# Kernel tuning notes

Hardware: AMD Instinct MI355X
Metric: run time of the kernel (lower is better)

Reference implementation:

```python
import jax, jax.numpy as jnp
import numpy as np

FP8_MAX = 448.0  # float8_e4m3fn max representable magnitude


def _fp8_quant_dequant(x, axis=-1):
    # Per-token (last-axis) dynamic scaling to e4m3, then dequantize back.
    scale = jnp.max(jnp.abs(x), axis=axis, keepdims=True) / FP8_MAX
    scale = jnp.maximum(scale, 1e-12)
    q = (x / scale).astype(jnp.float8_e4m3fn).astype(jnp.float32)
    return q * scale


def setup_inputs() -> dict:
    key = jax.random.key(0)
    k1, k2, k3, k4 = jax.random.split(key, 4)
    S, H, D, T = 64, 64, 128, 32768
    index_q = jax.random.normal(k1, (S, H, D), dtype=jnp.float32)
    index_k = jax.random.normal(k2, (T, D), dtype=jnp.float32)
    weights = jax.random.uniform(k3, (S, H), dtype=jnp.float32)
    cu_seqlen_ks = jnp.zeros((S,), dtype=jnp.int32)
    cu_seqlen_ke = jax.random.randint(k4, (S,), 1, T + 1, dtype=jnp.int32)
    return {
        "index_q": index_q,
        "index_k": index_k,
        "weights": weights,
        "cu_seqlen_ks": cu_seqlen_ks,
        "cu_seqlen_ke": cu_seqlen_ke,
    }


def reference(index_q, index_k, weights, cu_seqlen_ks, cu_seqlen_ke):
    # FP8 (e4m3) quantize-dequantize with per-token dynamic scales.
    q = _fp8_quant_dequant(index_q, axis=-1)   # [S, H, D]
    k = _fp8_quant_dequant(index_k, axis=-1)   # [T, D]
    # Index scores: relu(q.k) weighted-summed over heads -> [S, T]
    scores = jax.nn.relu(jnp.einsum("shd,td->sht", q, k))
    logits = jnp.einsum("sht,sh->st", scores, weights)
    # Ragged KV masking: query s sees kv tokens in [ks[s], ke[s]).
    t = jnp.arange(k.shape[0], dtype=jnp.int32)
    mask = (t[None, :] >= cu_seqlen_ks[:, None]) & (t[None, :] < cu_seqlen_ke[:, None])
    return jnp.where(mask, logits, -jnp.inf)
```

## Files before the change

kernel.cpp:

```cpp
#include <hip/hip_runtime.h>
#include <stdint.h>
#include <math.h>

#define NS 64
#define NH 64
#define ND 128
#define NT 32768
#define TN 256

#define MASK_VAL (-3.0e38f)

typedef __attribute__((ext_vector_type(4))) float f32x4;

__device__ __align__(16) uint8_t g_q8[NS * NH * ND];
__device__ __align__(16) uint8_t g_k8[NT * ND];
__device__ float g_wq[NS * NH];
__device__ float g_sk[NT];

__device__ __forceinline__ float wave_reduce_max(float m) {
#pragma unroll
  for (int off = 32; off >= 1; off >>= 1)
    m = fmaxf(m, __shfl_xor(m, off, 64));
  return m;
}

__device__ __forceinline__ uint32_t f32_to_e4m3(float x) {
  uint32_t u = __float_as_uint(x);
  uint32_t sign = (u >> 24) & 0x80u;
  uint32_t a = u & 0x7FFFFFFFu;
  if (a > 0x43E00000u) a = 0x43E00000u;
  uint32_t e = a >> 23;
  uint32_t code;
  if (e >= 121u) {
    uint32_t m = a & 0x7FFFFFu;
    m += 0x7FFFFu + ((m >> 20) & 1u);
    uint32_t carry = m >> 23;
    code = ((e - 120u + carry) << 3) | (carry ? 0u : ((m >> 20) & 7u));
    if (code > 0x7Eu) code = 0x7Eu;
  } else {
    code = (uint32_t)(int)rintf(__uint_as_float(a) * 512.0f);
  }
  return sign | code;
}

__global__ __launch_bounds__(256) void quant_q_kernel(
    const float* __restrict__ in, const float* __restrict__ weights) {
  int row = blockIdx.x * 4 + (threadIdx.x >> 6);
  int l = threadIdx.x & 63;
  float2 v = reinterpret_cast<const float2*>(in)[(size_t)row * 64 + l];
  float m = wave_reduce_max(fmaxf(fabsf(v.x), fabsf(v.y)));
  float scale = fmaxf(m / 448.0f, 1e-12f);
  uint32_t b0 = f32_to_e4m3(v.x / scale);
  uint32_t b1 = f32_to_e4m3(v.y / scale);
  reinterpret_cast<uint16_t*>(g_q8)[(size_t)row * 64 + l] =
      (uint16_t)(b0 | (b1 << 8));
  if (l == 0) g_wq[row] = weights[row] * scale;
}

__global__ __launch_bounds__(256) void quant_k_kernel(
    const float* __restrict__ in) {
  int row = blockIdx.x * 4 + (threadIdx.x >> 6);
  int l = threadIdx.x & 63;
  float2 v = reinterpret_cast<const float2*>(in)[(size_t)row * 64 + l];
  float m = wave_reduce_max(fmaxf(fabsf(v.x), fabsf(v.y)));
  float scale = fmaxf(m / 448.0f, 1e-12f);
  uint32_t b0 = f32_to_e4m3(v.x / scale);
  uint32_t b1 = f32_to_e4m3(v.y / scale);
  reinterpret_cast<uint16_t*>(g_k8)[(size_t)row * 64 + l] =
      (uint16_t)(b0 | (b1 << 8));
  if (l == 0) g_sk[row] = scale;
}

__global__ __launch_bounds__(256) void indexer_main_kernel(
    const int* __restrict__ ksA, const int* __restrict__ keA,
    float* __restrict__ out) {
  const int s = blockIdx.y;
  const int t0 = blockIdx.x * TN;
  const int ks = ksA[s], ke = keA[s];
  const int tid = threadIdx.x;

  if (t0 >= ke || t0 + TN <= ks) {
    out[(size_t)s * NT + t0 + tid] = MASK_VAL;
    return;
  }

  __shared__ __align__(16) uint8_t qs[NH * ND];
  __shared__ __align__(16) uint8_t ksm[TN * ND];
  __shared__ float wqs[NH];

#pragma unroll
  for (int i = 0; i < 2; ++i) {
    int idx = tid + i * 256;
    int row = idx >> 3, ch = idx & 7;
    int4 v = reinterpret_cast<const int4*>(g_q8 + (size_t)(s * NH + row) * ND)[ch];
    *reinterpret_cast<int4*>(&qs[row * ND + ((ch * 16) ^ ((row & 7) << 4))]) = v;
  }
#pragma unroll
  for (int i = 0; i < 8; ++i) {
    int idx = tid + i * 256;
    int row = idx >> 3, ch = idx & 7;
    int4 v = reinterpret_cast<const int4*>(g_k8 + (size_t)(t0 + row) * ND)[ch];
    *reinterpret_cast<int4*>(&ksm[row * ND + ((ch * 16) ^ ((row & 7) << 4))]) = v;
  }
  if (tid < NH) wqs[tid] = g_wq[s * NH + tid];
  __syncthreads();

  const int l = tid & 63;
  const int w = tid >> 6;
  const int col = l & 15;
  const int g = l >> 4;
  const int tw = w * 64;

  f32x4 acc[4][4];
  const f32x4 z = {0.f, 0.f, 0.f, 0.f};
#pragma unroll
  for (int i = 0; i < 4; ++i)
#pragma unroll
    for (int j = 0; j < 4; ++j) acc[i][j] = z;

#pragma unroll
  for (int kc = 0; kc < 4; ++kc) {
    const int k0 = kc * 32 + g * 8;
    long a[4], b[4];
#pragma unroll
    for (int ht = 0; ht < 4; ++ht) {
      int row = ht * 16 + col;
      a[ht] = *reinterpret_cast<const long*>(
          &qs[row * ND + (k0 ^ ((row & 7) << 4))]);
    }
#pragma unroll
    for (int tt = 0; tt < 4; ++tt) {
      int row = tw + tt * 16 + col;
      b[tt] = *reinterpret_cast<const long*>(
          &ksm[row * ND + (k0 ^ ((row & 7) << 4))]);
    }
#pragma unroll
    for (int ht = 0; ht < 4; ++ht)
#pragma unroll
      for (int tt = 0; tt < 4; ++tt)
        acc[ht][tt] = __builtin_amdgcn_mfma_f32_16x16x32_fp8_fp8(
            a[ht], b[tt], acc[ht][tt], 0, 0, 0);
  }

  float r[4];
#pragma unroll
  for (int tt = 0; tt < 4; ++tt) {
    float p = 0.f;
#pragma unroll
    for (int ht = 0; ht < 4; ++ht) {
#pragma unroll
      for (int j = 0; j < 4; ++j) {
        p += wqs[ht * 16 + g * 4 + j] * fmaxf(acc[ht][tt][j], 0.f);
      }
    }
    p += __shfl_xor(p, 16, 64);
    p += __shfl_xor(p, 32, 64);
    r[tt] = p;
  }
  float val = (g == 0) ? r[0] : (g == 1) ? r[1] : (g == 2) ? r[2] : r[3];
  const int t = t0 + tw + l;
  val *= g_sk[t];
  if (((__float_as_uint(val) >> 23) & 0xFFu) == 0xFFu) val = 0.0f;
  out[(size_t)s * NT + t] = (t >= ks && t < ke) ? val : MASK_VAL;
}

extern "C" void kernel_launch(void* const* d_in, const int* in_sizes, int n_in,
                              void* d_out, int out_size, void* d_ws, size_t ws_size,
                              hipStream_t stream) {
  (void)in_sizes; (void)n_in; (void)out_size; (void)d_ws; (void)ws_size;
  const float* index_q = (const float*)d_in[0];
  const float* index_k = (const float*)d_in[1];
  const float* weights = (const float*)d_in[2];
  const int* ksA = (const int*)d_in[3];
  const int* keA = (const int*)d_in[4];
  float* out = (float*)d_out;

  quant_q_kernel<<<dim3((NS * NH) / 4), 256, 0, stream>>>(index_q, weights);
  quant_k_kernel<<<dim3(NT / 4), 256, 0, stream>>>(index_k);
  indexer_main_kernel<<<dim3(NT / TN, NS), 256, 0, stream>>>(ksA, keA, out);
}
```

Measured before the change: 42.90 us.

## Batch sorted query rows per block to reuse K tile across queries

Adds a small kernel that sorts the query rows by their ke value, then has each main-kernel block process SB=4 queries with similar lengths for one 256-token K tile. The K tile is loaded into shared memory once, and the B fragments are kept in registers across the queries, which cuts K-tile reloads by a factor of four. Grouping by ke keeps wasted work on masked queries small, and a wave skips its compute when its 64 tokens are fully masked. The cost is 32KB more shared memory per block, which may lower occupancy, plus fewer blocks and one extra kernel launch.

```diff
diff --git a/kernel.cpp b/kernel.cpp
--- a/kernel.cpp
+++ b/kernel.cpp
@@ -7,6 +7,7 @@
 #define ND 128
 #define NT 32768
 #define TN 256
+#define SB 4
 
 #define MASK_VAL (-3.0e38f)
 
@@ -16,6 +17,7 @@
 __device__ __align__(16) uint8_t g_k8[NT * ND];
 __device__ float g_wq[NS * NH];
 __device__ float g_sk[NT];
+__device__ int   g_perm[NS];
 
 __device__ __forceinline__ float wave_reduce_max(float m) {
 #pragma unroll
@@ -71,30 +73,47 @@
   if (l == 0) g_sk[row] = scale;
 }
 
+__global__ void sort_ke_kernel(const int* __restrict__ keA) {
+  int l = threadIdx.x;
+  int ke = keA[l];
+  int rank = 0;
+#pragma unroll
+  for (int o = 0; o < NS; ++o) {
+    int keo = __shfl(ke, o, 64);
+    rank += (keo > ke) || (keo == ke && o < l);
+  }
+  g_perm[rank] = l;
+}
+
 __global__ __launch_bounds__(256) void indexer_main_kernel(
     const int* __restrict__ ksA, const int* __restrict__ keA,
     float* __restrict__ out) {
-  const int s = blockIdx.y;
-  const int t0 = blockIdx.x * TN;
-  const int ks = ksA[s], ke = keA[s];
+  const int sg = blockIdx.x;
+  const int t0 = blockIdx.y * TN;
   const int tid = threadIdx.x;
 
-  if (t0 >= ke || t0 + TN <= ks) {
-    out[(size_t)s * NT + t0 + tid] = MASK_VAL;
+  int sIdx[SB], ksv[SB], kev[SB];
+  bool act[SB];
+  bool any = false;
+#pragma unroll
+  for (int si = 0; si < SB; ++si) {
+    sIdx[si] = g_perm[sg * SB + si];
+    ksv[si] = ksA[sIdx[si]];
+    kev[si] = keA[sIdx[si]];
+    act[si] = (t0 < kev[si]) && (t0 + TN > ksv[si]);
+    any |= act[si];
+  }
+  if (!any) {
+#pragma unroll
+    for (int si = 0; si < SB; ++si)
+      out[(size_t)sIdx[si] * NT + t0 + tid] = MASK_VAL;
     return;
   }
 
-  __shared__ __align__(16) uint8_t qs[NH * ND];
   __shared__ __align__(16) uint8_t ksm[TN * ND];
-  __shared__ float wqs[NH];
-
-#pragma unroll
-  for (int i = 0; i < 2; ++i) {
-    int idx = tid + i * 256;
-    int row = idx >> 3, ch = idx & 7;
-    int4 v = reinterpret_cast<const int4*>(g_q8 + (size_t)(s * NH + row) * ND)[ch];
-    *reinterpret_cast<int4*>(&qs[row * ND + ((ch * 16) ^ ((row & 7) << 4))]) = v;
-  }
+  __shared__ __align__(16) uint8_t qs[SB * NH * ND];
+  __shared__ float wqs[SB * NH];
+
 #pragma unroll
   for (int i = 0; i < 8; ++i) {
     int idx = tid + i * 256;
@@ -102,7 +121,19 @@
     int4 v = reinterpret_cast<const int4*>(g_k8 + (size_t)(t0 + row) * ND)[ch];
     *reinterpret_cast<int4*>(&ksm[row * ND + ((ch * 16) ^ ((row & 7) << 4))]) = v;
   }
-  if (tid < NH) wqs[tid] = g_wq[s * NH + tid];
+#pragma unroll
+  for (int i = 0; i < 8; ++i) {
+    int idx = tid + i * 256;
+    int si = idx >> 9, row = (idx >> 3) & 63, ch = idx & 7;
+    int4 v = reinterpret_cast<const int4*>(
+        g_q8 + (size_t)(sIdx[si] * NH + row) * ND)[ch];
+    *reinterpret_cast<int4*>(
+        &qs[si * (NH * ND) + row * ND + ((ch * 16) ^ ((row & 7) << 4))]) = v;
+  }
+  {
+    int si = tid >> 6, h = tid & 63;
+    wqs[tid] = g_wq[sIdx[si] * NH + h];
+  }
   __syncthreads();
 
   const int l = tid & 63;
@@ -110,58 +141,71 @@
   const int col = l & 15;
   const int g = l >> 4;
   const int tw = w * 64;
-
-  f32x4 acc[4][4];
-  const f32x4 z = {0.f, 0.f, 0.f, 0.f};
-#pragma unroll
-  for (int i = 0; i < 4; ++i)
-#pragma unroll
-    for (int j = 0; j < 4; ++j) acc[i][j] = z;
-
-#pragma unroll
-  for (int kc = 0; kc < 4; ++kc) {
-    const int k0 = kc * 32 + g * 8;
-    long a[4], b[4];
-#pragma unroll
-    for (int ht = 0; ht < 4; ++ht) {
-      int row = ht * 16 + col;
-      a[ht] = *reinterpret_cast<const long*>(
-          &qs[row * ND + (k0 ^ ((row & 7) << 4))]);
-    }
+  const int wt0 = t0 + tw;
+
+  long b[4][4];
+#pragma unroll
+  for (int kc = 0; kc < 4; ++kc)
 #pragma unroll
     for (int tt = 0; tt < 4; ++tt) {
       int row = tw + tt * 16 + col;
-      b[tt] = *reinterpret_cast<const long*>(
-          &ksm[row * ND + (k0 ^ ((row & 7) << 4))]);
-    }
-#pragma unroll
-    for (int ht = 0; ht < 4; ++ht)
-#pragma unroll
-      for (int tt = 0; tt < 4; ++tt)
-        acc[ht][tt] = __builtin_amdgcn_mfma_f32_16x16x32_fp8_fp8(
-            a[ht], b[tt], acc[ht][tt], 0, 0, 0);
-  }
-
-  float r[4];
-#pragma unroll
-  for (int tt = 0; tt < 4; ++tt) {
-    float p = 0.f;
-#pragma unroll
-    for (int ht = 0; ht < 4; ++ht) {
-#pragma unroll
-      for (int j = 0; j < 4; ++j) {
-        p += wqs[ht * 16 + g * 4 + j] * fmaxf(acc[ht][tt][j], 0.f);
+      b[kc][tt] = *reinterpret_cast<const long*>(
+          &ksm[row * ND + ((kc * 32 + g * 8) ^ ((col & 7) << 4))]);
+    }
+
+  float skv = g_sk[wt0 + l];
+
+#pragma unroll
+  for (int si = 0; si < SB; ++si) {
+    const int s = sIdx[si];
+    if (wt0 >= kev[si] || wt0 + 64 <= ksv[si]) {
+      out[(size_t)s * NT + wt0 + l] = MASK_VAL;
+      continue;
+    }
+    f32x4 acc[4][4];
+    const f32x4 z = {0.f, 0.f, 0.f, 0.f};
+#pragma unroll
+    for (int i = 0; i < 4; ++i)
+#pragma unroll
+      for (int j = 0; j < 4; ++j) acc[i][j] = z;
+
+#pragma unroll
+    for (int kc = 0; kc < 4; ++kc) {
+      long a[4];
+#pragma unroll
+      for (int ht = 0; ht < 4; ++ht) {
+        int row = ht * 16 + col;
+        a[ht] = *reinterpret_cast<const long*>(
+            &qs[si * (NH * ND) + row * ND +
+                ((kc * 32 + g * 8) ^ ((col & 7) << 4))]);
       }
-    }
-    p += __shfl_xor(p, 16, 64);
-    p += __shfl_xor(p, 32, 64);
-    r[tt] = p;
-  }
-  float val = (g == 0) ? r[0] : (g == 1) ? r[1] : (g == 2) ? r[2] : r[3];
-  const int t = t0 + tw + l;
-  val *= g_sk[t];
-  if (((__float_as_uint(val) >> 23) & 0xFFu) == 0xFFu) val = 0.0f;
-  out[(size_t)s * NT + t] = (t >= ks && t < ke) ? val : MASK_VAL;
+#pragma unroll
+      for (int ht = 0; ht < 4; ++ht)
+#pragma unroll
+        for (int tt = 0; tt < 4; ++tt)
+          acc[ht][tt] = __builtin_amdgcn_mfma_f32_16x16x32_fp8_fp8(
+              a[ht], b[kc][tt], acc[ht][tt], 0, 0, 0);
+    }
+
+    float r[4];
+#pragma unroll
+    for (int tt = 0; tt < 4; ++tt) {
+      float p = 0.f;
+#pragma unroll
+      for (int ht = 0; ht < 4; ++ht)
+#pragma unroll
+        for (int j = 0; j < 4; ++j)
+          p += wqs[si * NH + ht * 16 + g * 4 + j] * fmaxf(acc[ht][tt][j], 0.f);
+      p += __shfl_xor(p, 16, 64);
+      p += __shfl_xor(p, 32, 64);
+      r[tt] = p;
+    }
+    float val = (g == 0) ? r[0] : (g == 1) ? r[1] : (g == 2) ? r[2] : r[3];
+    const int t = wt0 + l;
+    val *= skv;
+    if (((__float_as_uint(val) >> 23) & 0xFFu) == 0xFFu) val = 0.0f;
+    out[(size_t)s * NT + t] = (t >= ksv[si] && t < kev[si]) ? val : MASK_VAL;
+  }
 }
 
 extern "C" void kernel_launch(void* const* d_in, const int* in_sizes, int n_in,
@@ -177,5 +221,6 @@
 
   quant_q_kernel<<<dim3((NS * NH) / 4), 256, 0, stream>>>(index_q, weights);
   quant_k_kernel<<<dim3(NT / 4), 256, 0, stream>>>(index_k);
-  indexer_main_kernel<<<dim3(NT / TN, NS), 256, 0, stream>>>(ksA, keA, out);
-}
+  sort_ke_kernel<<<dim3(1), 64, 0, stream>>>(keA);
+  indexer_main_kernel<<<dim3(NS / SB, NT / TN), 256, 0, stream>>>(ksA, keA, out);
+}
```

Result: slower. 58.01 us (+35.2%).

## Drop LDS staging, load FP8 operands directly to registers, widen per-block span

Applied to the files above, without the earlier changes.

The main kernel no longer stages Q and K tiles in shared memory or calls __syncthreads. Each wave loads its MFMA operands straight from global memory, keeps Q fragments and weights in registers, and loops over a 1024-token span with per-wave skipping of masked 64-token chunks. The grid is transposed so blocks for the same query row are adjacent. The quant kernels now process 4 floats per lane with 32 lanes per row. This removes LDS traffic and barriers and skips work at wave granularity, at the cost of uncoalesced 8-byte global loads and less parallelism per block.

```diff
diff --git a/kernel.cpp b/kernel.cpp
--- a/kernel.cpp
+++ b/kernel.cpp
@@ -6,7 +6,7 @@
 #define NH 64
 #define ND 128
 #define NT 32768
-#define TN 256
+#define CHSPAN 1024
 
 #define MASK_VAL (-3.0e38f)
 
@@ -14,15 +14,8 @@
 
 __device__ __align__(16) uint8_t g_q8[NS * NH * ND];
 __device__ __align__(16) uint8_t g_k8[NT * ND];
-__device__ float g_wq[NS * NH];
-__device__ float g_sk[NT];
-
-__device__ __forceinline__ float wave_reduce_max(float m) {
-#pragma unroll
-  for (int off = 32; off >= 1; off >>= 1)
-    m = fmaxf(m, __shfl_xor(m, off, 64));
-  return m;
-}
+__device__ __align__(16) float g_wq[NS * NH];
+__device__ __align__(16) float g_sk[NT];
 
 __device__ __forceinline__ uint32_t f32_to_e4m3(float x) {
   uint32_t u = __float_as_uint(x);
@@ -43,125 +36,122 @@
   return sign | code;
 }
 
-__global__ __launch_bounds__(256) void quant_q_kernel(
-    const float* __restrict__ in, const float* __restrict__ weights) {
-  int row = blockIdx.x * 4 + (threadIdx.x >> 6);
-  int l = threadIdx.x & 63;
-  float2 v = reinterpret_cast<const float2*>(in)[(size_t)row * 64 + l];
-  float m = wave_reduce_max(fmaxf(fabsf(v.x), fabsf(v.y)));
+__device__ __forceinline__ void quant_row4(
+    const float* __restrict__ in, uint8_t* __restrict__ q8out,
+    float* __restrict__ scale_out, const float* __restrict__ wmul,
+    int row, int c) {
+  float4 v = reinterpret_cast<const float4*>(in)[(size_t)row * 32 + c];
+  float m = fmaxf(fmaxf(fabsf(v.x), fabsf(v.y)), fmaxf(fabsf(v.z), fabsf(v.w)));
+#pragma unroll
+  for (int off = 16; off >= 1; off >>= 1)
+    m = fmaxf(m, __shfl_xor(m, off, 64));
   float scale = fmaxf(m / 448.0f, 1e-12f);
   uint32_t b0 = f32_to_e4m3(v.x / scale);
   uint32_t b1 = f32_to_e4m3(v.y / scale);
-  reinterpret_cast<uint16_t*>(g_q8)[(size_t)row * 64 + l] =
-      (uint16_t)(b0 | (b1 << 8));
-  if (l == 0) g_wq[row] = weights[row] * scale;
+  uint32_t b2 = f32_to_e4m3(v.z / scale);
+  uint32_t b3 = f32_to_e4m3(v.w / scale);
+  reinterpret_cast<uint32_t*>(q8out)[(size_t)row * 32 + c] =
+      b0 | (b1 << 8) | (b2 << 16) | (b3 << 24);
+  if (c == 0) scale_out[row] = wmul ? wmul[row] * scale : scale;
+}
+
+__global__ __launch_bounds__(256) void quant_q_kernel(
+    const float* __restrict__ in, const float* __restrict__ weights) {
+  quant_row4(in, g_q8, g_wq, weights,
+             blockIdx.x * 8 + (threadIdx.x >> 5), threadIdx.x & 31);
 }
 
 __global__ __launch_bounds__(256) void quant_k_kernel(
     const float* __restrict__ in) {
-  int row = blockIdx.x * 4 + (threadIdx.x >> 6);
-  int l = threadIdx.x & 63;
-  float2 v = reinterpret_cast<const float2*>(in)[(size_t)row * 64 + l];
-  float m = wave_reduce_max(fmaxf(fabsf(v.x), fabsf(v.y)));
-  float scale = fmaxf(m / 448.0f, 1e-12f);
-  uint32_t b0 = f32_to_e4m3(v.x / scale);
-  uint32_t b1 = f32_to_e4m3(v.y / scale);
-  reinterpret_cast<uint16_t*>(g_k8)[(size_t)row * 64 + l] =
-      (uint16_t)(b0 | (b1 << 8));
-  if (l == 0) g_sk[row] = scale;
+  quant_row4(in, g_k8, g_sk, nullptr,
+             blockIdx.x * 8 + (threadIdx.x >> 5), threadIdx.x & 31);
 }
 
 __global__ __launch_bounds__(256) void indexer_main_kernel(
     const int* __restrict__ ksA, const int* __restrict__ keA,
     float* __restrict__ out) {
-  const int s = blockIdx.y;
-  const int t0 = blockIdx.x * TN;
+  const int s = blockIdx.x;
+  const int c0 = blockIdx.y * CHSPAN;
   const int ks = ksA[s], ke = keA[s];
   const int tid = threadIdx.x;
+  float* orow = out + (size_t)s * NT;
 
-  if (t0 >= ke || t0 + TN <= ks) {
-    out[(size_t)s * NT + t0 + tid] = MASK_VAL;
+  if (c0 >= ke || c0 + CHSPAN <= ks) {
+#pragma unroll
+    for (int i = 0; i < CHSPAN / 256; ++i)
+      orow[c0 + i * 256 + tid] = MASK_VAL;
     return;
   }
-
-  __shared__ __align__(16) uint8_t qs[NH * ND];
-  __shared__ __align__(16) uint8_t ksm[TN * ND];
-  __shared__ float wqs[NH];
-
-#pragma unroll
-  for (int i = 0; i < 2; ++i) {
-    int idx = tid + i * 256;
-    int row = idx >> 3, ch = idx & 7;
-    int4 v = reinterpret_cast<const int4*>(g_q8 + (size_t)(s * NH + row) * ND)[ch];
-    *reinterpret_cast<int4*>(&qs[row * ND + ((ch * 16) ^ ((row & 7) << 4))]) = v;
-  }
-#pragma unroll
-  for (int i = 0; i < 8; ++i) {
-    int idx = tid + i * 256;
-    int row = idx >> 3, ch = idx & 7;
-    int4 v = reinterpret_cast<const int4*>(g_k8 + (size_t)(t0 + row) * ND)[ch];
-    *reinterpret_cast<int4*>(&ksm[row * ND + ((ch * 16) ^ ((row & 7) << 4))]) = v;
-  }
-  if (tid < NH) wqs[tid] = g_wq[s * NH + tid];
-  __syncthreads();
 
   const int l = tid & 63;
   const int w = tid >> 6;
   const int col = l & 15;
   const int g = l >> 4;
-  const int tw = w * 64;
 
-  f32x4 acc[4][4];
-  const f32x4 z = {0.f, 0.f, 0.f, 0.f};
+  long a[4][4];
 #pragma unroll
-  for (int i = 0; i < 4; ++i)
+  for (int kc = 0; kc < 4; ++kc)
 #pragma unroll
-    for (int j = 0; j < 4; ++j) acc[i][j] = z;
+    for (int ht = 0; ht < 4; ++ht)
+      a[kc][ht] = *reinterpret_cast<const long*>(
+          g_q8 + ((size_t)s * NH + ht * 16 + col) * ND + kc * 32 + g * 8);
+
+  float4 wq4[4];
+#pragma unroll
+  for (int ht = 0; ht < 4; ++ht)
+    wq4[ht] = *reinterpret_cast<const float4*>(g_wq + s * NH + ht * 16 + g * 4);
 
 #pragma unroll
-  for (int kc = 0; kc < 4; ++kc) {
-    const int k0 = kc * 32 + g * 8;
-    long a[4], b[4];
+  for (int i = 0; i < CHSPAN / 256; ++i) {
+    const int t0w = c0 + i * 256 + w * 64;
+    const int t = t0w + l;
+    if (t0w >= ke || t0w + 64 <= ks) {
+      orow[t] = MASK_VAL;
+      continue;
+    }
+
+    f32x4 acc[4][4];
+    const f32x4 z = {0.f, 0.f, 0.f, 0.f};
 #pragma unroll
-    for (int ht = 0; ht < 4; ++ht) {
-      int row = ht * 16 + col;
-      a[ht] = *reinterpret_cast<const long*>(
-          &qs[row * ND + (k0 ^ ((row & 7) << 4))]);
+    for (int x = 0; x < 4; ++x)
+#pragma unroll
+      for (int y = 0; y < 4; ++y) acc[x][y] = z;
+
+#pragma unroll
+    for (int kc = 0; kc < 4; ++kc) {
+      long b[4];
+#pragma unroll
+      for (int tt = 0; tt < 4; ++tt)
+        b[tt] = *reinterpret_cast<const long*>(
+            g_k8 + ((size_t)(t0w + tt * 16 + col)) * ND + kc * 32 + g * 8);
+#pragma unroll
+      for (int ht = 0; ht < 4; ++ht)
+#pragma unroll
+        for (int tt = 0; tt < 4; ++tt)
+          acc[ht][tt] = __builtin_amdgcn_mfma_f32_16x16x32_fp8_fp8(
+              a[kc][ht], b[tt], acc[ht][tt], 0, 0, 0);
     }
+
+    float r[4];
 #pragma unroll
     for (int tt = 0; tt < 4; ++tt) {
-      int row = tw + tt * 16 + col;
-      b[tt] = *reinterpret_cast<const long*>(
-          &ksm[row * ND + (k0 ^ ((row & 7) << 4))]);
+      float p = 0.f;
+#pragma unroll
+      for (int ht = 0; ht < 4; ++ht) {
+        p += wq4[ht].x * fmaxf(acc[ht][tt][0], 0.f);
+        p += wq4[ht].y * fmaxf(acc[ht][tt][1], 0.f);
+        p += wq4[ht].z * fmaxf(acc[ht][tt][2], 0.f);
+        p += wq4[ht].w * fmaxf(acc[ht][tt][3], 0.f);
+      }
+      p += __shfl_xor(p, 16, 64);
+      p += __shfl_xor(p, 32, 64);
+      r[tt] = p;
     }
-#pragma unroll
-    for (int ht = 0; ht < 4; ++ht)
-#pragma unroll
-      for (int tt = 0; tt < 4; ++tt)
-        acc[ht][tt] = __builtin_amdgcn_mfma_f32_16x16x32_fp8_fp8(
-            a[ht], b[tt], acc[ht][tt], 0, 0, 0);
+    float val = (g == 0) ? r[0] : (g == 1) ? r[1] : (g == 2) ? r[2] : r[3];
+    val *= g_sk[t];
+    if (((__float_as_uint(val) >> 23) & 0xFFu) == 0xFFu) val = 0.0f;
+    orow[t] = (t >= ks && t < ke) ? val : MASK_VAL;
   }
-
-  float r[4];
-#pragma unroll
-  for (int tt = 0; tt < 4; ++tt) {
-    float p = 0.f;
-#pragma unroll
-    for (int ht = 0; ht < 4; ++ht) {
-#pragma unroll
-      for (int j = 0; j < 4; ++j) {
-        p += wqs[ht * 16 + g * 4 + j] * fmaxf(acc[ht][tt][j], 0.f);
-      }
-    }
-    p += __shfl_xor(p, 16, 64);
-    p += __shfl_xor(p, 32, 64);
-    r[tt] = p;
-  }
-  float val = (g == 0) ? r[0] : (g == 1) ? r[1] : (g == 2) ? r[2] : r[3];
-  const int t = t0 + tw + l;
-  val *= g_sk[t];
-  if (((__float_as_uint(val) >> 23) & 0xFFu) == 0xFFu) val = 0.0f;
-  out[(size_t)s * NT + t] = (t >= ks && t < ke) ? val : MASK_VAL;
 }
 
 extern "C" void kernel_launch(void* const* d_in, const int* in_sizes, int n_in,
@@ -175,7 +165,7 @@
   const int* keA = (const int*)d_in[4];
   float* out = (float*)d_out;
 
-  quant_q_kernel<<<dim3((NS * NH) / 4), 256, 0, stream>>>(index_q, weights);
-  quant_k_kernel<<<dim3(NT / 4), 256, 0, stream>>>(index_k);
-  indexer_main_kernel<<<dim3(NT / TN, NS), 256, 0, stream>>>(ksA, keA, out);
+  quant_q_kernel<<<dim3((NS * NH) / 8), 256, 0, stream>>>(index_q, weights);
+  quant_k_kernel<<<dim3(NT / 8), 256, 0, stream>>>(index_k);
+  indexer_main_kernel<<<dim3(NS, NT / CHSPAN), 256, 0, stream>>>(ksA, keA, out);
 }
```

After: 92.06 us. +114.6%, slower.
